# Optimization experiments

Hardware: AMD Instinct MI355X
Metric: run time of the kernel (lower is better)

Reference implementation:

```python
import jax, jax.numpy as jnp
import numpy as np

LAMBDA_COORD = 5.0
LAMBDA_NOOBJ = 0.5
B, A, C, G = 64, 10647, 9, 50


def setup_inputs() -> dict:
    key = jax.random.key(0)
    k1, k2, k3, k4 = jax.random.split(key, 4)
    # pred: boxes (cx,cy,w,h) + conf + 9 class probs; conf/cls must be in (0,1) for BCE
    pred = jax.random.uniform(k1, (B, A, 5 + C), dtype=jnp.float32) * 0.98 + 0.01
    # GT boxes in corner format (x1,y1,x2,y2), normalized
    xy1 = jax.random.uniform(k2, (B, G, 2), dtype=jnp.float32) * 0.7
    wh = jax.random.uniform(k3, (B, G, 2), dtype=jnp.float32) * 0.25 + 0.02
    bboxes = jnp.concatenate([xy1, xy1 + wh], axis=-1)
    classes = jax.random.randint(k4, (B, G), 0, C, dtype=jnp.int64 if jax.config.jax_enable_x64 else jnp.int32)
    classes = classes.at[:, 40:].set(-1)   # padding slots
    classes = classes.at[0].set(-1)        # one image with no GT (empty-image path)
    return {"pred": pred, "bboxes": bboxes, "classes": classes}


def _clamp_log(x):
    # torch BCELoss clamps each log term to >= -100
    return jnp.maximum(jnp.log(x), -100.0)


def _yolo_loss(pred, bboxes, classes):
    n_batch = pred.shape[0]
    n_cls = pred.shape[-1] - 5
    pred_boxes = pred[..., :4]      # [B, A, 4] (cx, cy, w, h)
    pred_conf = pred[..., 4]        # [B, A]
    pred_cls = pred[..., 5:]        # [B, A, C]

    valid = classes != -1           # [B, G]

    # GT corners -> yolo (cx, cy, w, h)
    gt_cx = (bboxes[..., 0] + bboxes[..., 2]) / 2
    gt_cy = (bboxes[..., 1] + bboxes[..., 3]) / 2
    gt_w = bboxes[..., 2] - bboxes[..., 0]
    gt_h = bboxes[..., 3] - bboxes[..., 1]
    gt_yolo = jnp.stack([gt_cx, gt_cy, gt_w, gt_h], axis=-1)  # [B, G, 4]

    # IoU of every anchor vs every GT (both cxcywh), broadcast: [B, G, A]
    p = pred_boxes[:, None, :, :]   # [B, 1, A, 4]
    g = gt_yolo[:, :, None, :]      # [B, G, 1, 4]
    p_x1 = p[..., 0] - p[..., 2] / 2; p_y1 = p[..., 1] - p[..., 3] / 2
    p_x2 = p[..., 0] + p[..., 2] / 2; p_y2 = p[..., 1] + p[..., 3] / 2
    g_x1 = g[..., 0] - g[..., 2] / 2; g_y1 = g[..., 1] - g[..., 3] / 2
    g_x2 = g[..., 0] + g[..., 2] / 2; g_y2 = g[..., 1] + g[..., 3] / 2
    iw = jnp.clip(jnp.minimum(p_x2, g_x2) - jnp.maximum(p_x1, g_x1), 0.0)
    ih = jnp.clip(jnp.minimum(p_y2, g_y2) - jnp.maximum(p_y1, g_y1), 0.0)
    inter = iw * ih
    area_p = (p_x2 - p_x1) * (p_y2 - p_y1)
    area_g = (g_x2 - g_x1) * (g_y2 - g_y1)
    iou = inter / (area_p + area_g - inter + 1e-16)   # [B, G, A]

    best = jnp.argmax(iou, axis=-1)                    # [B, G]

    pb_best = jnp.take_along_axis(pred_boxes, best[:, :, None], axis=1)   # [B, G, 4]
    pc_best = jnp.take_along_axis(pred_conf, best, axis=1)                # [B, G]
    pcls_best = jnp.take_along_axis(pred_cls, best[:, :, None], axis=1)   # [B, G, C]

    # coordinate MSE (sum over x,y,w,h)
    coord = LAMBDA_COORD * jnp.sum((pb_best - gt_yolo) ** 2, axis=-1)     # [B, G]
    # objectness BCE vs 1 at best anchor
    conf_obj = -_clamp_log(pc_best)                                        # [B, G]
    # class BCE vs one-hot
    onehot = jax.nn.one_hot(classes, n_cls, dtype=pred.dtype)              # [B, G, C]
    cls_loss = -jnp.sum(onehot * _clamp_log(pcls_best)
                        + (1.0 - onehot) * _clamp_log(1.0 - pcls_best), axis=-1)
    # no-obj BCE: per GT, sum over all anchors except best of -log(1-conf)
    bce0 = -_clamp_log(1.0 - pred_conf)                                    # [B, A]
    tot0 = jnp.sum(bce0, axis=-1)                                          # [B]
    bce0_best = jnp.take_along_axis(bce0, best, axis=1)                    # [B, G]
    noobj = LAMBDA_NOOBJ * (tot0[:, None] - bce0_best)

    per_gt = coord + conf_obj + cls_loss + noobj
    per_img = jnp.sum(jnp.where(valid, per_gt, 0.0), axis=-1)              # [B]
    has_gt = jnp.any(valid, axis=-1)
    per_img = jnp.where(has_gt, per_img, LAMBDA_NOOBJ * tot0)
    return jnp.sum(per_img) / n_batch


def reference(pred, bboxes, classes):
    return _yolo_loss(pred, bboxes, classes)
```

## Files before the change

### kernel.cpp

```cpp
#include <hip/hip_runtime.h>

#define LAMBDA_COORD 5.0f
#define LAMBDA_NOOBJ 0.5f

constexpr int Bn = 64;
constexpr int An = 10647;
constexpr int Cn = 9;
constexpr int Gn = 50;
constexpr int PRED_ROW = 5 + Cn;
constexpr int S  = 16;
constexpr int AC = (An + S - 1) / S;


__global__ __launch_bounds__(256) void yolo_k1(
    const float* __restrict__ pred,
    const float* __restrict__ bboxes,
    float2* __restrict__ partials,
    float* __restrict__ bcepart)
{
    const int s = blockIdx.x;
    const int b = blockIdx.y;
    const int a0 = s * AC;
    const int a1 = min(a0 + AC, An);
    const int n  = a1 - a0;

    __shared__ float4 sbox[AC];
    __shared__ float  sap[AC];
    __shared__ float  sred[4];

    const int tid  = threadIdx.x;
    const int wave = tid >> 6;
    const int lane = tid & 63;

    const float* prow = pred + (size_t)b * An * PRED_ROW;
    float bce = 0.0f;
    for (int i = tid; i < n; i += 256) {
        const float* p = prow + (size_t)(a0 + i) * PRED_ROW;
        float cx = p[0], cy = p[1], w = p[2], h = p[3], conf = p[4];
        float hw = 0.5f * w, hh = 0.5f * h;
        float x1 = cx - hw, x2 = cx + hw;
        float y1 = cy - hh, y2 = cy + hh;
        sbox[i] = make_float4(x1, y1, x2, y2);
        sap[i]  = (x2 - x1) * (y2 - y1);
        bce -= fmaxf(__logf(1.0f - conf), -100.0f);
    }
    #pragma unroll
    for (int off = 32; off >= 1; off >>= 1) bce += __shfl_xor(bce, off, 64);
    if (lane == 0) sred[wave] = bce;
    __syncthreads();
    if (tid == 0) bcepart[b * S + s] = sred[0] + sred[1] + sred[2] + sred[3];

    const float* bb = bboxes + (size_t)b * Gn * 4;
    for (int g = wave; g < Gn; g += 4) {
        float b0 = bb[g * 4 + 0], b1 = bb[g * 4 + 1];
        float b2 = bb[g * 4 + 2], b3 = bb[g * 4 + 3];
        float gcx = 0.5f * (b0 + b2), gcy = 0.5f * (b1 + b3);
        float gw = b2 - b0, gh = b3 - b1;
        float gx1 = gcx - gw * 0.5f, gx2 = gcx + gw * 0.5f;
        float gy1 = gcy - gh * 0.5f, gy2 = gcy + gh * 0.5f;
        float c1 = (gx2 - gx1) * (gy2 - gy1) + 1e-16f;

        float best = -1.0f;
        int   bidx = 0x7fffffff;
        for (int i = lane; i < n; i += 64) {
            float4 pb = sbox[i];
            float iw = fminf(pb.z, gx2) - fmaxf(pb.x, gx1);
            float ih = fminf(pb.w, gy2) - fmaxf(pb.y, gy1);
            iw = fmaxf(iw, 0.0f);
            ih = fmaxf(ih, 0.0f);
            float inter = iw * ih;
            float denom = (sap[i] + c1) - inter;
            float iou = inter * __builtin_amdgcn_rcpf(denom);
            if (iou > best) { best = iou; bidx = a0 + i; }
        }
        #pragma unroll
        for (int off = 1; off < 64; off <<= 1) {
            float oi  = __shfl_xor(best, off, 64);
            int   oix = __shfl_xor(bidx, off, 64);
            if (oi > best || (oi == best && oix < bidx)) { best = oi; bidx = oix; }
        }
        if (lane == 0)
            partials[((size_t)b * Gn + g) * S + s] = make_float2(best, __int_as_float(bidx));
    }
}

__global__ __launch_bounds__(64) void yolo_k2(
    const float* __restrict__ pred,
    const float* __restrict__ bboxes,
    const int*  __restrict__ classes,
    const float2* __restrict__ partials,
    const float* __restrict__ bcepart,
    float* __restrict__ per_img)
{
    const int b = blockIdx.x;
    const int g = threadIdx.x;

    float tot0 = 0.0f;
    #pragma unroll
    for (int s = 0; s < S; ++s) tot0 += bcepart[b * S + s];

    float per_gt = 0.0f;
    int   validf = 0;
    if (g < Gn) {
        int cls = classes[b * Gn + g];
        validf = (cls != -1) ? 1 : 0;

        const float2* pp = partials + ((size_t)b * Gn + g) * S;
        float best = -1.0f;
        int   bidx = 0x7fffffff;
        #pragma unroll
        for (int s = 0; s < S; ++s) {
            float2 c = pp[s];
            float ci = c.x;
            int   cx = __float_as_int(c.y);
            if (ci > best || (ci == best && cx < bidx)) { best = ci; bidx = cx; }
        }

        const float* p = pred + ((size_t)b * An + bidx) * PRED_ROW;
        float pcx = p[0], pcy = p[1], pw = p[2], ph = p[3], conf = p[4];

        const float* bb = bboxes + ((size_t)b * Gn + g) * 4;
        float b0 = bb[0], b1 = bb[1], b2 = bb[2], b3 = bb[3];
        float gcx = 0.5f * (b0 + b2), gcy = 0.5f * (b1 + b3);
        float gw = b2 - b0, gh = b3 - b1;

        float dx = pcx - gcx, dy = pcy - gcy, dw = pw - gw, dh = ph - gh;
        float coord = LAMBDA_COORD * (dx * dx + dy * dy + dw * dw + dh * dh);

        float conf_obj = -fmaxf(__logf(conf), -100.0f);

        float clsl = 0.0f;
        #pragma unroll
        for (int c = 0; c < Cn; ++c) {
            float pc = p[5 + c];
            float lp = fmaxf(__logf(pc), -100.0f);
            float ln = fmaxf(__logf(1.0f - pc), -100.0f);
            clsl -= (c == cls) ? lp : ln;
        }

        float bce0b = -fmaxf(__logf(1.0f - conf), -100.0f);
        float noobj = LAMBDA_NOOBJ * (tot0 - bce0b);

        per_gt = coord + conf_obj + clsl + noobj;
        if (!validf) per_gt = 0.0f;
    }

    float sum = per_gt;
    int   anyv = validf;
    #pragma unroll
    for (int off = 1; off < 64; off <<= 1) {
        sum  += __shfl_xor(sum, off, 64);
        anyv |= __shfl_xor(anyv, off, 64);
    }
    if (g == 0) per_img[b] = anyv ? sum : (LAMBDA_NOOBJ * tot0);
}

__global__ __launch_bounds__(64) void yolo_k3(
    const float* __restrict__ per_img, float* __restrict__ out)
{
    float v = per_img[threadIdx.x];
    #pragma unroll
    for (int off = 1; off < 64; off <<= 1) v += __shfl_xor(v, off, 64);
    if (threadIdx.x == 0) out[0] = v * (1.0f / (float)Bn);
}

extern "C" void kernel_launch(void* const* d_in, const int* in_sizes, int n_in,
                              void* d_out, int out_size, void* d_ws, size_t ws_size,
                              hipStream_t stream) {
    const float* pred    = (const float*)d_in[0];
    const float* bboxes  = (const float*)d_in[1];
    const int*   classes = (const int*)d_in[2];
    float* out = (float*)d_out;

    char* ws = (char*)d_ws;
    float2* partials = (float2*)ws;
    float*  bcepart  = (float*)(ws + (size_t)Bn * Gn * S * sizeof(float2));
    float*  per_img  = (float*)(ws + (size_t)Bn * Gn * S * sizeof(float2)
                                   + (size_t)Bn * S * sizeof(float));

    yolo_k1<<<dim3(S, Bn), 256, 0, stream>>>(pred, bboxes, partials, bcepart);
    yolo_k2<<<Bn, 64, 0, stream>>>(pred, bboxes, classes, partials, bcepart, per_img);
    yolo_k3<<<1, 64, 0, stream>>>(per_img, out);
}
```

Measured before the change: 117.2 us.

## Register-block GT boxes per wave and compare IoU by cross-multiplication

Each wave now keeps 13 GT boxes in registers and makes a single pass over the shared-memory anchor boxes. Every anchor load is reused across all 13 GTs, where the old code re-read the anchors from LDS once per GT. The per-anchor reciprocal is replaced by a cross-multiplied comparison of inter/denominator fractions, with only one rcp per GT at the end. Tie-breaking changes: lowest-index preference in the shuffle and cross-block reductions is dropped, so exact ties may pick a different anchor than argmax. Register pressure also rises a lot.

```diff
diff --git a/kernel.cpp b/kernel.cpp
--- a/kernel.cpp
+++ b/kernel.cpp
@@ -10,6 +10,7 @@
 constexpr int PRED_ROW = 5 + Cn;
 constexpr int S  = 16;
 constexpr int AC = (An + S - 1) / S;
+constexpr int GTW = 13;
 
 
 __global__ __launch_bounds__(256) void yolo_k1(
@@ -21,8 +22,7 @@
     const int s = blockIdx.x;
     const int b = blockIdx.y;
     const int a0 = s * AC;
-    const int a1 = min(a0 + AC, An);
-    const int n  = a1 - a0;
+    const int n  = min(AC, An - a0);
 
     __shared__ float4 sbox[AC];
     __shared__ float  sap[AC];
@@ -47,40 +47,69 @@
     #pragma unroll
     for (int off = 32; off >= 1; off >>= 1) bce += __shfl_xor(bce, off, 64);
     if (lane == 0) sred[wave] = bce;
-    __syncthreads();
-    if (tid == 0) bcepart[b * S + s] = sred[0] + sred[1] + sred[2] + sred[3];
-
+
+    const int g0 = wave * GTW;
+    const int ng = min(GTW, Gn - g0);
+
+    float gx1[GTW], gy1[GTW], gx2[GTW], gy2[GTW], gc1[GTW];
     const float* bb = bboxes + (size_t)b * Gn * 4;
-    for (int g = wave; g < Gn; g += 4) {
+    #pragma unroll
+    for (int j = 0; j < GTW; ++j) {
+        int g = (j < ng) ? (g0 + j) : g0;
         float b0 = bb[g * 4 + 0], b1 = bb[g * 4 + 1];
         float b2 = bb[g * 4 + 2], b3 = bb[g * 4 + 3];
         float gcx = 0.5f * (b0 + b2), gcy = 0.5f * (b1 + b3);
         float gw = b2 - b0, gh = b3 - b1;
-        float gx1 = gcx - gw * 0.5f, gx2 = gcx + gw * 0.5f;
-        float gy1 = gcy - gh * 0.5f, gy2 = gcy + gh * 0.5f;
-        float c1 = (gx2 - gx1) * (gy2 - gy1) + 1e-16f;
-
-        float best = -1.0f;
-        int   bidx = 0x7fffffff;
-        for (int i = lane; i < n; i += 64) {
+        gx1[j] = gcx - gw * 0.5f; gx2[j] = gcx + gw * 0.5f;
+        gy1[j] = gcy - gh * 0.5f; gy2[j] = gcy + gh * 0.5f;
+        gc1[j] = (gx2[j] - gx1[j]) * (gy2[j] - gy1[j]) + 1e-16f;
+    }
+
+    float bn[GTW], bd[GTW];
+    int   bidx[GTW];
+    #pragma unroll
+    for (int j = 0; j < GTW; ++j) { bn[j] = -1.0f; bd[j] = 1.0f; bidx[j] = 0; }
+
+    __syncthreads();
+    if (tid == 0) bcepart[b * S + s] = sred[0] + sred[1] + sred[2] + sred[3];
+
+    for (int base = 0; base < n; base += 64) {
+        int i = base + lane;
+        if (i < n) {
             float4 pb = sbox[i];
-            float iw = fminf(pb.z, gx2) - fmaxf(pb.x, gx1);
-            float ih = fminf(pb.w, gy2) - fmaxf(pb.y, gy1);
-            iw = fmaxf(iw, 0.0f);
-            ih = fmaxf(ih, 0.0f);
-            float inter = iw * ih;
-            float denom = (sap[i] + c1) - inter;
-            float iou = inter * __builtin_amdgcn_rcpf(denom);
-            if (iou > best) { best = iou; bidx = a0 + i; }
-        }
-        #pragma unroll
-        for (int off = 1; off < 64; off <<= 1) {
-            float oi  = __shfl_xor(best, off, 64);
-            int   oix = __shfl_xor(bidx, off, 64);
-            if (oi > best || (oi == best && oix < bidx)) { best = oi; bidx = oix; }
-        }
-        if (lane == 0)
-            partials[((size_t)b * Gn + g) * S + s] = make_float2(best, __int_as_float(bidx));
+            float  ap = sap[i];
+            int   idx = a0 + i;
+            #pragma unroll
+            for (int j = 0; j < GTW; ++j) {
+                float iw = fminf(pb.z, gx2[j]) - fmaxf(pb.x, gx1[j]);
+                float ih = fminf(pb.w, gy2[j]) - fmaxf(pb.y, gy1[j]);
+                iw = fmaxf(iw, 0.0f);
+                ih = fmaxf(ih, 0.0f);
+                float inter = iw * ih;
+                float apc   = ap + gc1[j];
+                bool take = inter * bd[j] > bn[j] * apc;
+                bn[j]   = take ? inter : bn[j];
+                bd[j]   = take ? apc   : bd[j];
+                bidx[j] = take ? idx   : bidx[j];
+            }
+        }
+    }
+
+    #pragma unroll
+    for (int j = 0; j < GTW; ++j) {
+        if (j < ng) {
+            float score = bn[j] * __builtin_amdgcn_rcpf(bd[j]);
+            int   idx   = bidx[j];
+            #pragma unroll
+            for (int off = 1; off < 64; off <<= 1) {
+                float os = __shfl_xor(score, off, 64);
+                int   oi = __shfl_xor(idx, off, 64);
+                if (os > score) { score = os; idx = oi; }
+            }
+            if (lane == 0)
+                partials[((size_t)b * Gn + g0 + j) * S + s] =
+                    make_float2(score, __int_as_float(idx));
+        }
     }
 }
 
@@ -107,13 +136,11 @@
 
         const float2* pp = partials + ((size_t)b * Gn + g) * S;
         float best = -1.0f;
-        int   bidx = 0x7fffffff;
+        int   bidx = 0;
         #pragma unroll
         for (int s = 0; s < S; ++s) {
             float2 c = pp[s];
-            float ci = c.x;
-            int   cx = __float_as_int(c.y);
-            if (ci > best || (ci == best && cx < bidx)) { best = ci; bidx = cx; }
+            if (c.x > best) { best = c.x; bidx = __float_as_int(c.y); }
         }
 
         const float* p = pred + ((size_t)b * An + bidx) * PRED_ROW;
```

New measurement: 107.9 us. 1.09x faster.
